# Optimization experiments

Hardware: AMD Instinct MI355X
Metric: run time of the kernel (lower is better)

Reference implementation:

```python
import jax, jax.numpy as jnp
import numpy as np

SEQ, HID = 4096, 1024
NEG_INF = -10000000000.0


def setup_inputs() -> dict:
    key = jax.random.key(0)
    ks = jax.random.split(key, 6)
    s = 1.0 / np.sqrt(HID)
    return {
        "query": jax.random.normal(ks[0], (SEQ, HID), jnp.float32),
        "key": jax.random.normal(ks[1], (SEQ, HID), jnp.float32),
        "value": jax.random.normal(ks[2], (SEQ, HID), jnp.float32),
        # SASRec causal mask: allowed positions are 1, masked are 0
        "mask": jnp.tril(jnp.ones((SEQ, SEQ), jnp.int32)),
        "Wq": jax.random.normal(ks[3], (HID, HID), jnp.float32) * s,
        "Wk": jax.random.normal(ks[4], (HID, HID), jnp.float32) * s,
        "Wv": jax.random.normal(ks[5], (HID, HID), jnp.float32) * s,
    }


def reference(query, key, value, mask, Wq, Wk, Wv):
    # nn.Linear(bias=False): y = x @ W.T
    Q = query @ Wq.T   # [S, H]
    K = key @ Wk.T     # [S, H]
    V = value @ Wv.T   # [S, H]
    scale = jnp.sqrt(jnp.asarray(HID, Q.dtype))
    energy = (Q @ K.T) / scale                      # [S, S]
    energy = jnp.where(mask == 0, NEG_INF, energy)  # masked_fill
    attention = jax.nn.softmax(energy, axis=-1)     # [S, S]
    x = attention @ V                               # dropout is identity in eval
    return (x, attention)
```

## Files before the change

kernel.cpp:

```cpp
#include <hip/hip_runtime.h>

#define SEQ 4096
#define HID 1024

typedef _Float16 f16x4 __attribute__((ext_vector_type(4)));
typedef _Float16 f16x8 __attribute__((ext_vector_type(8)));
typedef float    f32x4 __attribute__((ext_vector_type(4)));

__device__ __forceinline__ void gld16(const void* g, void* l) {
    __builtin_amdgcn_global_load_lds(
        (const __attribute__((address_space(1))) unsigned int*)g,
        (__attribute__((address_space(3))) unsigned int*)l, 16, 0, 0);
}

__global__ __launch_bounds__(256) void cast_all(
    const float4* __restrict__ q, const float4* __restrict__ k,
    const float4* __restrict__ v,
    const float4* __restrict__ wq, const float4* __restrict__ wk,
    const float4* __restrict__ wv,
    f16x4* __restrict__ qh, f16x4* __restrict__ kh, f16x4* __restrict__ vh,
    f16x4* __restrict__ wqh, f16x4* __restrict__ wkh, f16x4* __restrict__ wvh,
    int nX4, int nW4) {
    int t = blockIdx.x * 256 + threadIdx.x;
    const float4 *a, *b, *c; f16x4 *da, *db, *dc; int idx;
    if (t < nX4) { a = q; b = k; c = v; da = qh; db = kh; dc = vh; idx = t; }
    else if (t < nX4 + nW4) {
        idx = t - nX4;
        a = wq; b = wk; c = wv; da = wqh; db = wkh; dc = wvh;
    } else return;
    float4 va = a[idx], vb = b[idx], vc = c[idx];
    f16x4 oa = {(_Float16)va.x, (_Float16)va.y, (_Float16)va.z, (_Float16)va.w};
    f16x4 ob = {(_Float16)vb.x, (_Float16)vb.y, (_Float16)vb.z, (_Float16)vb.w};
    f16x4 oc = {(_Float16)vc.x, (_Float16)vc.y, (_Float16)vc.z, (_Float16)vc.w};
    da[idx] = oa; db[idx] = ob; dc[idx] = oc;
}

template <typename OutT, bool TRI_SKIP, bool TRI_K, int ZMODE>
__global__ __launch_bounds__(256) void gemm_nt(
    const _Float16* __restrict__ A, const _Float16* __restrict__ Bt,
    OutT* __restrict__ C, int M, int N, int K, float scale,
    long sA, long sB, long sC, int KC, float* __restrict__ PB,
    const _Float16* __restrict__ A2, const _Float16* __restrict__ B2,
    OutT* __restrict__ C2, int N2) {
    __shared__ __attribute__((aligned(16))) _Float16 As[2 * 128 * 32];
    __shared__ __attribute__((aligned(16))) _Float16 Bs[2 * 128 * 32];

    int bm = blockIdx.y;
    int bn = blockIdx.x;
    if (TRI_SKIP && bn > bm) return;
    const _Float16* Ap = A;
    const _Float16* Bp = Bt;
    OutT* Cp = C;
    int Nloc = N;
    if (ZMODE == 7) {
        if (blockIdx.z < 2) {
            Ap = A  + (long)blockIdx.z * sA;
            Bp = Bt + (long)blockIdx.z * sB;
            Cp = C  + (long)blockIdx.z * sC;
        } else {
            Ap = A2; Bp = B2; Cp = C2; Nloc = N2;
            bm = blockIdx.x; bn = blockIdx.y;
        }
    }

    int kstart = 0, kend, zslot = -1;
    if (ZMODE == 4) {
        const int y = 79 - (int)blockIdx.y;
        int g = 0;
        while (4 * (g + 1) * (g + 2) <= y) ++g;
        const int rem = y - 4 * g * (g + 1);
        const int m   = g + 1;
        const int rg  = rem / m;
        bm = 8 * g + rg;
        const int z = rem - rg * m;
        kstart = z * KC;
        kend   = min((bm + 1) * 128, kstart + KC);
        if (z > 0) zslot = 4 * g * (g - 1) + rg * g + (z - 1);
    } else if (ZMODE == 5) {
        kstart = blockIdx.z * KC;
        kend   = kstart + KC;
        Cp += (long)blockIdx.z * sC;
    } else {
        kend = TRI_K ? min(K, (bm + 1) * 128) : K;
    }

    const int tid = threadIdx.x;
    const int tr  = tid >> 2;
    const int tc8 = (tid & 3) * 8;

    const _Float16* Ab = Ap + (size_t)bm * 128 * K;
    const _Float16* Bb = Bp + (size_t)bn * 128 * K;

    const int wave = tid >> 6;
    const int lane = tid & 63;
    const int wm = (wave >> 1) * 64;
    const int wn = (wave & 1) * 64;
    const int lr = lane & 15;
    const int lk = (lane >> 4) * 8;

    f32x4 acc[4][4];
#pragma unroll
    for (int i = 0; i < 4; ++i)
#pragma unroll
        for (int j = 0; j < 4; ++j) acc[i][j] = (f32x4)0.0f;

    for (int k0 = kstart; k0 < kend; k0 += 64) {
#pragma unroll
        for (int h = 0; h < 2; ++h) {
            const int kk = k0 + h * 32, off = h * 4096;
            gld16(Ab + (size_t)tr * K        + kk + tc8, &As[off + tr * 32 + tc8]);
            gld16(Ab + (size_t)(64 + tr) * K + kk + tc8, &As[off + (64 + tr) * 32 + tc8]);
            gld16(Bb + (size_t)tr * K        + kk + tc8, &Bs[off + tr * 32 + tc8]);
            gld16(Bb + (size_t)(64 + tr) * K + kk + tc8, &Bs[off + (64 + tr) * 32 + tc8]);
        }
        __syncthreads();

#pragma unroll
        for (int h = 0; h < 2; ++h) {
            const int off = h * 4096;
            f16x8 af[4], bfr[4];
#pragma unroll
            for (int i = 0; i < 4; ++i)
                af[i] = *(const f16x8*)&As[off + (wm + i * 16 + lr) * 32 + lk];
#pragma unroll
            for (int j = 0; j < 4; ++j)
                bfr[j] = *(const f16x8*)&Bs[off + (wn + j * 16 + lr) * 32 + lk];
#pragma unroll
            for (int i = 0; i < 4; ++i)
#pragma unroll
                for (int j = 0; j < 4; ++j)
                    acc[i][j] = __builtin_amdgcn_mfma_f32_16x16x32_f16(
                        af[i], bfr[j], acc[i][j], 0, 0, 0);
        }
        __syncthreads();
    }

    const int er = (lane >> 4) * 4;
    const int ec = lane & 15;
#pragma unroll
    for (int i = 0; i < 4; ++i) {
#pragma unroll
        for (int j = 0; j < 4; ++j) {
            const int lrow0 = wm + i * 16 + er;
            const int col   = bn * 128 + wn + j * 16 + ec;
#pragma unroll
            for (int r = 0; r < 4; ++r) {
                const float val = acc[i][j][r] * scale;
                if (ZMODE == 4 && zslot >= 0)
                    PB[(size_t)(zslot * 128 + lrow0 + r) * 1024 + col] = val;
                else
                    Cp[(long)(bm * 128 + lrow0 + r) * Nloc + col] = (OutT)val;
            }
        }
    }
}

__global__ __launch_bounds__(256) void reduce_pv(
    float* __restrict__ out, const float* __restrict__ PB) {
    const int row = 1024 + blockIdx.x;
    const int bm  = row >> 7;
    const int g   = bm >> 3;
    const int slot0 = 4 * g * (g - 1) + (bm - 8 * g) * g;
    const int rloc  = row & 127;
    float4* o = (float4*)(out + (size_t)row * 1024) + threadIdx.x;
    float4 acc = *o;
    for (int z = 0; z < g; ++z) {
        const float4 p = *((const float4*)(PB +
            ((size_t)(slot0 + z) * 128 + rloc) * 1024) + threadIdx.x);
        acc.x += p.x; acc.y += p.y; acc.z += p.z; acc.w += p.w;
    }
    *o = acc;
}

__global__ __launch_bounds__(256) void softmax_causal(
    _Float16* __restrict__ EP0, const _Float16* __restrict__ EP1,
    float* __restrict__ att, int S) {
    __shared__ float rowbuf[SEQ];
    __shared__ float red[8];
    const int i   = blockIdx.x;
    const int tid = threadIdx.x;
    const int wv  = tid >> 6, ln = tid & 63;
    _Float16* E0row = EP0 + (size_t)i * S;
    const _Float16* E1row = EP1 + (size_t)i * S;

    float lmax = -INFINITY;
    for (int j8 = tid * 8; j8 <= i; j8 += 2048) {
        f16x8 a8 = *(const f16x8*)&E0row[j8];
        f16x8 b8 = *(const f16x8*)&E1row[j8];
#pragma unroll
        for (int u = 0; u < 8; ++u) {
            int j = j8 + u;
            if (j <= i) {
                float vv = (float)a8[u] + (float)b8[u];
                rowbuf[j] = vv;
                lmax = fmaxf(lmax, vv);
            }
        }
    }
#pragma unroll
    for (int o = 32; o > 0; o >>= 1) lmax = fmaxf(lmax, __shfl_down(lmax, o, 64));
    if (ln == 0) red[wv] = lmax;
    __syncthreads();
    if (tid == 0)
        red[4] = fmaxf(fmaxf(red[0], red[1]), fmaxf(red[2], red[3]));
    __syncthreads();
    const float rmax = red[4];

    float lsum = 0.0f;
    for (int j4 = tid * 4; j4 <= i; j4 += 1024) {
        float4 e = *(float4*)&rowbuf[j4];
        float4 o;
        o.x = (j4     <= i) ? __expf(e.x - rmax) : 0.f;
        o.y = (j4 + 1 <= i) ? __expf(e.y - rmax) : 0.f;
        o.z = (j4 + 2 <= i) ? __expf(e.z - rmax) : 0.f;
        o.w = (j4 + 3 <= i) ? __expf(e.w - rmax) : 0.f;
        *(float4*)&rowbuf[j4] = o;
        lsum += o.x + o.y + o.z + o.w;
    }
#pragma unroll
    for (int o = 32; o > 0; o >>= 1) lsum += __shfl_down(lsum, o, 64);
    __syncthreads();
    if (ln == 0) red[wv] = lsum;
    __syncthreads();
    if (tid == 0)
        red[4] = red[0] + red[1] + red[2] + red[3];
    __syncthreads();
    const float rinv = 1.0f / red[4];

    float* arow = att + (size_t)i * S;
    const int jlim = ((i >> 7) + 1) << 7;
    for (int j4 = tid * 4; j4 < S; j4 += 1024) {
        float4 a;
        a.x = (j4     <= i) ? rowbuf[j4]     * rinv : 0.f;
        a.y = (j4 + 1 <= i) ? rowbuf[j4 + 1] * rinv : 0.f;
        a.z = (j4 + 2 <= i) ? rowbuf[j4 + 2] * rinv : 0.f;
        a.w = (j4 + 3 <= i) ? rowbuf[j4 + 3] * rinv : 0.f;
        *(float4*)&arow[j4] = a;
        if (j4 < jlim) {
            f16x4 p = {(_Float16)a.x, (_Float16)a.y, (_Float16)a.z, (_Float16)a.w};
            *(f16x4*)&E0row[j4] = p;
        }
    }
}

extern "C" void kernel_launch(void* const* d_in, const int* in_sizes, int n_in,
                              void* d_out, int out_size, void* d_ws, size_t ws_size,
                              hipStream_t stream) {
    const float* q  = (const float*)d_in[0];
    const float* k  = (const float*)d_in[1];
    const float* v  = (const float*)d_in[2];
    const float* Wq = (const float*)d_in[4];
    const float* Wk = (const float*)d_in[5];
    const float* Wv = (const float*)d_in[6];

    float* out_x   = (float*)d_out;
    float* out_att = out_x + (size_t)SEQ * HID;

    char* ws = (char*)d_ws;
    const size_t SH = (size_t)SEQ * HID * sizeof(_Float16);
    const size_t HH = (size_t)HID * HID * sizeof(_Float16);
    _Float16* qh  = (_Float16*)(ws);
    _Float16* vh  = (_Float16*)(ws + SH);
    _Float16* wqh = (_Float16*)(ws + 2 * SH);
    _Float16* wkh = (_Float16*)(ws + 2 * SH + HH);
    _Float16* wvh = (_Float16*)(ws + 2 * SH + 2 * HH);
    _Float16* EP1 = (_Float16*)(ws);
    _Float16* kh  = (_Float16*)(ws + 4 * SH);
    _Float16* Qh  = (_Float16*)(ws + 5 * SH);
    _Float16* Kh  = (_Float16*)(ws + 6 * SH);
    _Float16* VT  = (_Float16*)(ws + 7 * SH);
    _Float16* EP0 = (_Float16*)(ws + 8 * SH);
    float* Pbuf = (float*)ws;

    const int nX4 = SEQ * HID / 4, nW4 = HID * HID / 4;
    cast_all<<<(nX4 + nW4 + 255) / 256, 256, 0, stream>>>(
        (const float4*)q, (const float4*)k, (const float4*)v,
        (const float4*)Wq, (const float4*)Wk, (const float4*)Wv,
        (f16x4*)qh, (f16x4*)kh, (f16x4*)vh,
        (f16x4*)wqh, (f16x4*)wkh, (f16x4*)wvh, nX4, nW4);

    gemm_nt<_Float16, false, false, 7><<<dim3(HID / 128, SEQ / 128, 3), 256, 0, stream>>>(
        qh, wqh, Qh, SEQ, HID, HID, 1.0f,
        (long)(kh - qh), (long)(wkh - wqh), (long)(Kh - Qh), 0, nullptr,
        wvh, vh, VT, SEQ);

    gemm_nt<_Float16, true, false, 5><<<dim3(SEQ / 128, SEQ / 128, 2), 256, 0, stream>>>(
        Qh, Kh, EP0, SEQ, SEQ, HID, 0.03125f,
        0, 0, (long)(EP1 - EP0), 512, nullptr, nullptr, nullptr, nullptr, 0);

    softmax_causal<<<SEQ, 256, 0, stream>>>(EP0, EP1, out_att, SEQ);

    gemm_nt<float, false, true, 4><<<dim3(HID / 128, 80), 256, 0, stream>>>(
        EP0, VT, out_x, SEQ, HID, SEQ, 1.0f, 0, 0, 0, 1024, Pbuf,
        nullptr, nullptr, nullptr, 0);

    reduce_pv<<<3072, 256, 0, stream>>>(out_x, Pbuf);
}
```

Baseline: 306.9 us.

## Double-buffer GEMM LDS tiles to overlap global loads with MFMA compute

Replaces the load-all-then-compute loop over 64-wide K chunks with a two-stage pipeline over 32-wide K slices. The next slice is prefetched into the alternate LDS buffer while MFMAs run on the current one, with explicit vmcnt waits and raw s_barrier calls in place of __syncthreads. This aims to hide global-to-LDS latency behind compute, at the cost of twice as many barriers per K and relying on hand-written waitcnt correctness for the LDS-direct loads.

```diff
diff --git a/kernel.cpp b/kernel.cpp
--- a/kernel.cpp
+++ b/kernel.cpp
@@ -104,36 +104,48 @@
 #pragma unroll
         for (int j = 0; j < 4; ++j) acc[i][j] = (f32x4)0.0f;
 
-    for (int k0 = kstart; k0 < kend; k0 += 64) {
-#pragma unroll
-        for (int h = 0; h < 2; ++h) {
-            const int kk = k0 + h * 32, off = h * 4096;
-            gld16(Ab + (size_t)tr * K        + kk + tc8, &As[off + tr * 32 + tc8]);
-            gld16(Ab + (size_t)(64 + tr) * K + kk + tc8, &As[off + (64 + tr) * 32 + tc8]);
-            gld16(Bb + (size_t)tr * K        + kk + tc8, &Bs[off + tr * 32 + tc8]);
-            gld16(Bb + (size_t)(64 + tr) * K + kk + tc8, &Bs[off + (64 + tr) * 32 + tc8]);
-        }
-        __syncthreads();
-
-#pragma unroll
-        for (int h = 0; h < 2; ++h) {
-            const int off = h * 4096;
-            f16x8 af[4], bfr[4];
-#pragma unroll
-            for (int i = 0; i < 4; ++i)
-                af[i] = *(const f16x8*)&As[off + (wm + i * 16 + lr) * 32 + lk];
+    #define STAGE(b, kk)                                                        \
+        do {                                                                    \
+            const int off_ = (b) * 4096;                                        \
+            gld16(Ab + (size_t)tr * K        + (kk) + tc8,                      \
+                  &As[off_ + tr * 32 + tc8]);                                   \
+            gld16(Ab + (size_t)(64 + tr) * K + (kk) + tc8,                      \
+                  &As[off_ + (64 + tr) * 32 + tc8]);                            \
+            gld16(Bb + (size_t)tr * K        + (kk) + tc8,                      \
+                  &Bs[off_ + tr * 32 + tc8]);                                   \
+            gld16(Bb + (size_t)(64 + tr) * K + (kk) + tc8,                      \
+                  &Bs[off_ + (64 + tr) * 32 + tc8]);                            \
+        } while (0)
+
+    const int nit = (kend - kstart) >> 5;
+    STAGE(0, kstart);
+    for (int it = 0; it < nit; ++it) {
+        const int cur = it & 1;
+        if (it + 1 < nit) {
+            STAGE(cur ^ 1, kstart + (it + 1) * 32);
+            asm volatile("s_waitcnt vmcnt(4)" ::: "memory");
+        } else {
+            asm volatile("s_waitcnt vmcnt(0)" ::: "memory");
+        }
+        __builtin_amdgcn_s_barrier();
+
+        const int off = cur * 4096;
+        f16x8 af[4], bfr[4];
+#pragma unroll
+        for (int i = 0; i < 4; ++i)
+            af[i] = *(const f16x8*)&As[off + (wm + i * 16 + lr) * 32 + lk];
+#pragma unroll
+        for (int j = 0; j < 4; ++j)
+            bfr[j] = *(const f16x8*)&Bs[off + (wn + j * 16 + lr) * 32 + lk];
+#pragma unroll
+        for (int i = 0; i < 4; ++i)
 #pragma unroll
             for (int j = 0; j < 4; ++j)
-                bfr[j] = *(const f16x8*)&Bs[off + (wn + j * 16 + lr) * 32 + lk];
-#pragma unroll
-            for (int i = 0; i < 4; ++i)
-#pragma unroll
-                for (int j = 0; j < 4; ++j)
-                    acc[i][j] = __builtin_amdgcn_mfma_f32_16x16x32_f16(
-                        af[i], bfr[j], acc[i][j], 0, 0, 0);
-        }
-        __syncthreads();
-    }
+                acc[i][j] = __builtin_amdgcn_mfma_f32_16x16x32_f16(
+                    af[i], bfr[j], acc[i][j], 0, 0, 0);
+        __builtin_amdgcn_s_barrier();
+    }
+    #undef STAGE
 
     const int er = (lane >> 4) * 4;
     const int ec = lane & 15;
```

After: 305.5 us. About the same (-0.4%).
